# Kernel optimization log

Hardware: AMD Instinct MI355X
Metric: run time of the kernel (lower is better)

## Reference

```python
import jax, jax.numpy as jnp
import numpy as np

# NVFP4 E2M1 representable magnitudes and decision midpoints (round-to-nearest)
_E2M1_GRID = np.array([0.0, 0.5, 1.0, 1.5, 2.0, 3.0, 4.0, 6.0], dtype=np.float32)
_E2M1_MIDS = np.array([0.25, 0.75, 1.25, 1.75, 2.5, 3.5, 5.0], dtype=np.float32)
_BLOCK = 16  # quant_tile_shape=(1,16)


def fake_quant_nvfp4(t):
    """Blockwise (16 contiguous elems) E2M1 fake quant with pow2 scales."""
    shape = t.shape
    v = t.reshape(-1, _BLOCK)                      # [n_blocks, 16]
    amax = jnp.max(jnp.abs(v), axis=-1, keepdims=True)
    # power-of-2 scale so that amax/scale <= 6 (E2M1 max)
    exp = jnp.ceil(jnp.log2(jnp.maximum(amax, jnp.float32(1e-30)) / 6.0))
    scale = jnp.where(amax > 0, jnp.exp2(exp), jnp.float32(1.0))
    u = v / scale
    a = jnp.abs(u)
    grid = jnp.asarray(_E2M1_GRID, dtype=t.dtype)
    mids = jnp.asarray(_E2M1_MIDS, dtype=t.dtype)
    idx = jnp.digitize(a, mids)                    # nearest E2M1 magnitude index
    q = jnp.sign(u) * grid[idx]
    return (q * scale).reshape(shape)


def setup_inputs() -> dict:
    key = jax.random.key(0)
    kx, kw = jax.random.split(key)
    x = jax.random.normal(kx, (32, 256, 64, 64), dtype=jnp.float32)
    w = jax.random.normal(kw, (256, 256, 3, 3), dtype=jnp.float32) * 0.05
    return {"x": x, "w": w}


def reference(x, w):
    qx = fake_quant_nvfp4(x)
    qw = fake_quant_nvfp4(w)
    # conv2d, stride 1, padding 1, no bias, NCHW / OIHW
    return jax.lax.conv_general_dilated(
        qx, qw,
        window_strides=(1, 1),
        padding=((1, 1), (1, 1)),
        dimension_numbers=("NCHW", "OIHW", "NCHW"),
    )
```

## Files before the change

kernel.cpp:

```cpp
#include <hip/hip_runtime.h>
#include <stdint.h>

typedef __attribute__((ext_vector_type(8))) short short8;
typedef __attribute__((ext_vector_type(4))) float f32x4;

#define N_IMG 32
#define C_IN  256
#define HH    64
#define WW    64
#define O_OUT 256
#define HP    66
#define WP    66

#define QX_ELEMS (N_IMG*HP*WP*C_IN)
#define QX_BYTES ((size_t)QX_ELEMS*2)
#define QW_ELEMS (9*O_OUT*C_IN)


__device__ __forceinline__ float e2m1_mag(float a) {
    return a < 0.25f ? 0.0f
         : a < 0.75f ? 0.5f
         : a < 1.25f ? 1.0f
         : a < 1.75f ? 1.5f
         : a < 2.5f  ? 2.0f
         : a < 3.5f  ? 3.0f
         : a < 5.0f  ? 4.0f : 6.0f;
}

__device__ __forceinline__ void blk_scale2(float amax, float& s, float& inv) {
    float ac = fmaxf(amax, 1e-30f);
    int e;
    float m = frexpf(ac, &e);
    int ex = (m > 0.75f) ? (e - 2) : (e - 3);
    if (amax > 0.0f) { s = ldexpf(1.0f, ex); inv = ldexpf(1.0f, -ex); }
    else             { s = 1.0f; inv = 1.0f; }
}

__device__ __forceinline__ unsigned short to_bf16_bits(float v) {
    union { float f; unsigned int u; } cv; cv.f = v;
    return (unsigned short)(cv.u >> 16);
}

__global__ __launch_bounds__(256) void halo_zero_kernel(unsigned short* __restrict__ qx) {
    int id = blockIdx.x * 256 + threadIdx.x;
    size_t off;
    if (id < 135168) {
        int n = id / 4224, r = id % 4224;
        int h = (r / 2112) * 65;
        int k = r % 2112;
        off = (((size_t)(n*HP + h)) * WP) * C_IN + (size_t)k * 8;
    } else {
        int j = id - 135168;
        int n = j >> 12, r = j & 4095;
        int h = 1 + (r >> 6);
        int w = ((r >> 5) & 1) * 65;
        int k = r & 31;
        off = (((size_t)(n*HP + h)) * WP + w) * C_IN + (size_t)k * 8;
    }
    uint4 z; z.x = z.y = z.z = z.w = 0u;
    *(uint4*)(qx + off) = z;
}

__global__ __launch_bounds__(256) void quant_x_kernel(const float* __restrict__ x,
                                                      unsigned short* __restrict__ qx) {
    __shared__ float xf[64][65];
    __shared__ float sarr[4][65];
    __shared__ float iarr[4][65];

    const int bid = blockIdx.x;
    const int n  = bid >> 8;
    const int h  = (bid >> 2) & 63;
    const int cb = bid & 3;
    const int t  = threadIdx.x;

    {
        const int rb = t >> 4;
        const int w4 = (t & 15) * 4;
        const float* src = x + (((size_t)(n*C_IN + cb*64)) * HH + h) * WW;
#pragma unroll
        for (int it = 0; it < 4; ++it) {
            int r = it * 16 + rb;
            float4 g = *(const float4*)(src + (size_t)r * (HH*WW) + w4);
            xf[r][w4+0] = g.x; xf[r][w4+1] = g.y; xf[r][w4+2] = g.z; xf[r][w4+3] = g.w;
        }
    }
    __syncthreads();

    {
        const int c = t >> 2, wb = t & 3;
        float amax = 0.f;
#pragma unroll
        for (int j = 0; j < 16; ++j) amax = fmaxf(amax, fabsf(xf[c][wb*16 + j]));
        float s, inv;
        blk_scale2(amax, s, inv);
        sarr[wb][c] = s;
        iarr[wb][c] = inv;
    }
    __syncthreads();

    {
        const int w = t >> 2, cg = (t & 3) * 16, wb = w >> 4;
        unsigned short outv[16];
#pragma unroll
        for (int i = 0; i < 16; ++i) {
            int c = cg + i;
            float v = xf[c][w];
            float q = copysignf(e2m1_mag(fabsf(v) * iarr[wb][c]) * sarr[wb][c], v);
            outv[i] = to_bf16_bits(q);
        }
        unsigned short* dst = qx + (((size_t)(n*HP + h + 1)) * WP + (w + 1)) * C_IN + cb*64 + cg;
        *(uint4*)(dst)     = *(const uint4*)&outv[0];
        *(uint4*)(dst + 8) = *(const uint4*)&outv[8];
    }
}

__global__ __launch_bounds__(256) void quant_w_kernel(const float* __restrict__ w,
                                                      unsigned short* __restrict__ qw) {
    __shared__ unsigned short lq[2304];
    const int o = blockIdx.x;
    const int t = threadIdx.x;
    const float* src = w + (size_t)o * 2304;
    if (t < 144) {
        float v[16];
#pragma unroll
        for (int j = 0; j < 4; ++j) {
            float4 f = ((const float4*)(src + t*16))[j];
            v[j*4+0]=f.x; v[j*4+1]=f.y; v[j*4+2]=f.z; v[j*4+3]=f.w;
        }
        float amax = 0.f;
#pragma unroll
        for (int j = 0; j < 16; ++j) amax = fmaxf(amax, fabsf(v[j]));
        float s, inv;
        blk_scale2(amax, s, inv);
#pragma unroll
        for (int j = 0; j < 16; ++j)
            lq[t*16 + j] = to_bf16_bits(copysignf(e2m1_mag(fabsf(v[j]) * inv) * s, v[j]));
    }
    __syncthreads();
#pragma unroll
    for (int p = 0; p < 9; ++p)
        qw[((size_t)(p*O_OUT + o)) * C_IN + t] = lq[t*9 + p];
}

__device__ __forceinline__ void gld16(void* lds, const void* g) {
    __builtin_amdgcn_global_load_lds(
        (const __attribute__((address_space(1))) unsigned int*)g,
        (__attribute__((address_space(3))) unsigned int*)lds,
        16, 0, 0);
}

__global__ __launch_bounds__(256) void conv_kernel(const unsigned short* __restrict__ qw,
                                                   const unsigned short* __restrict__ qx,
                                                   float* __restrict__ out) {
    __shared__ unsigned short Wt[128][32];
    __shared__ unsigned short Xt[128][32];

    const int tid  = threadIdx.x;
    const int wave = tid >> 6;
    const int lane = tid & 63;
    const int lo16 = lane & 15;
    const int quad = lane >> 4;

    const int id  = blockIdx.x;
    const int g   = id >> 3;
    const int n   = ((g >> 6) << 3) | (id & 7);
    const int j_  = g & 63;
    const int o0  = (j_ & 1) * 128;
    const int hw0 = (j_ >> 1) * 128;
    const int h0  = hw0 >> 6;

    const int s0 = wave * 2;
    const int r0 = s0 * 16 + (lane >> 2);
    const int r1 = r0 + 16;
    const int co = (lane & 3) * 8;

    const unsigned short* wb0 = qw + (size_t)(o0 + r0) * C_IN + co;
    const unsigned short* wb1 = qw + (size_t)(o0 + r1) * C_IN + co;

    auto xbase = [&](int r) -> const unsigned short* {
        int h = h0 + (r >> 6);
        int w = r & 63;
        return qx + (((size_t)(n*HP + h + 1)) * WP + (w + 1)) * C_IN + co;
    };
    const unsigned short* xb0 = xbase(r0);
    const unsigned short* xb1 = xbase(r1);

    unsigned short* ldsA0 = &Wt[s0*16][0];
    unsigned short* ldsA1 = &Wt[s0*16 + 16][0];
    unsigned short* ldsB0 = &Xt[s0*16][0];
    unsigned short* ldsB1 = &Xt[s0*16 + 16][0];

    const int wmo = (wave & 1) * 64;
    const int wnp = (wave >> 1) * 64;

    f32x4 acc[4][4];
#pragma unroll
    for (int i = 0; i < 4; ++i)
#pragma unroll
        for (int j = 0; j < 4; ++j)
            acc[i][j] = (f32x4){0.f, 0.f, 0.f, 0.f};

    for (int p = 0; p < 9; ++p) {
        const int dh = p/3 - 1, dw = p%3 - 1;
        const int xoff = (dh*WP + dw) * C_IN;
        const int woff = p * (O_OUT * C_IN);
        for (int cc = 0; cc < 8; ++cc) {
            const int c0 = cc * 32;
            gld16(ldsA0, wb0 + woff + c0);
            gld16(ldsA1, wb1 + woff + c0);
            gld16(ldsB0, xb0 + xoff + c0);
            gld16(ldsB1, xb1 + xoff + c0);
            __syncthreads();

            short8 af[4], bf_[4];
#pragma unroll
            for (int i = 0; i < 4; ++i)
                af[i] = *(const short8*)&Wt[wmo + i*16 + lo16][quad*8];
#pragma unroll
            for (int j = 0; j < 4; ++j)
                bf_[j] = *(const short8*)&Xt[wnp + j*16 + lo16][quad*8];
#pragma unroll
            for (int i = 0; i < 4; ++i)
#pragma unroll
                for (int j = 0; j < 4; ++j)
                    acc[i][j] = __builtin_amdgcn_mfma_f32_16x16x32_bf16(
                        af[i], bf_[j], acc[i][j], 0, 0, 0);
            __syncthreads();
        }
    }

#pragma unroll
    for (int i = 0; i < 4; ++i) {
#pragma unroll
        for (int j = 0; j < 4; ++j) {
            int o  = o0 + wmo + i*16 + quad*4;
            int pl = wnp + j*16 + lo16;
            size_t base = ((size_t)(n*O_OUT + o)) * (HH*WW) + hw0 + pl;
#pragma unroll
            for (int r = 0; r < 4; ++r)
                out[base + (size_t)r*(HH*WW)] = acc[i][j][r];
        }
    }
}

extern "C" void kernel_launch(void* const* d_in, const int* in_sizes, int n_in,
                              void* d_out, int out_size, void* d_ws, size_t ws_size,
                              hipStream_t stream) {
    const float* x = (const float*)d_in[0];
    const float* w = (const float*)d_in[1];
    float* out = (float*)d_out;

    unsigned short* qx = (unsigned short*)d_ws;
    unsigned short* qw = (unsigned short*)((char*)d_ws + QX_BYTES);

    halo_zero_kernel<<<dim3(1040), 256, 0, stream>>>(qx);
    quant_x_kernel<<<dim3(N_IMG*HH*4), 256, 0, stream>>>(x, qx);
    quant_w_kernel<<<dim3(O_OUT), 256, 0, stream>>>(w, qw);
    conv_kernel<<<dim3(2048), 256, 0, stream>>>(qw, qx, out);
}
```

Measured before the change: 433.4 us.

## Double-buffer X tile in LDS, load weights directly to registers, swizzle LDS

Measured after the change: 543.0 us. 25.3% more time.

```diff
diff --git a/kernel.cpp b/kernel.cpp
--- a/kernel.cpp
+++ b/kernel.cpp
@@ -139,7 +139,7 @@
     __syncthreads();
 #pragma unroll
     for (int p = 0; p < 9; ++p)
-        qw[((size_t)(p*O_OUT + o)) * C_IN + t] = lq[t*9 + p];
+        qw[(size_t)o*2304 + p*C_IN + t] = lq[t*9 + p];
 }
 
 __device__ __forceinline__ void gld16(void* lds, const void* g) {
@@ -152,8 +152,7 @@
 __global__ __launch_bounds__(256) void conv_kernel(const unsigned short* __restrict__ qw,
                                                    const unsigned short* __restrict__ qx,
                                                    float* __restrict__ out) {
-    __shared__ unsigned short Wt[128][32];
-    __shared__ unsigned short Xt[128][32];
+    __shared__ unsigned short Xb[2][128][32];
 
     const int tid  = threadIdx.x;
     const int wave = tid >> 6;
@@ -169,29 +168,25 @@
     const int hw0 = (j_ >> 1) * 128;
     const int h0  = hw0 >> 6;
 
-    const int s0 = wave * 2;
-    const int r0 = s0 * 16 + (lane >> 2);
+    const int r0 = wave*32 + (lane >> 2);
     const int r1 = r0 + 16;
-    const int co = (lane & 3) * 8;
-
-    const unsigned short* wb0 = qw + (size_t)(o0 + r0) * C_IN + co;
-    const unsigned short* wb1 = qw + (size_t)(o0 + r1) * C_IN + co;
-
-    auto xbase = [&](int r) -> const unsigned short* {
-        int h = h0 + (r >> 6);
-        int w = r & 63;
-        return qx + (((size_t)(n*HP + h + 1)) * WP + (w + 1)) * C_IN + co;
-    };
-    const unsigned short* xb0 = xbase(r0);
-    const unsigned short* xb1 = xbase(r1);
-
-    unsigned short* ldsA0 = &Wt[s0*16][0];
-    unsigned short* ldsA1 = &Wt[s0*16 + 16][0];
-    unsigned short* ldsB0 = &Xt[s0*16][0];
-    unsigned short* ldsB1 = &Xt[s0*16 + 16][0];
+    const int cl = (lane & 3) ^ ((lane >> 3) & 3);
+    const int co = cl * 8;
+
+    const unsigned short* xb0 = qx + (((size_t)(n*HP + h0 + (r0 >> 6) + 1))*WP + (r0 & 63) + 1)*C_IN + co;
+    const unsigned short* xb1 = qx + (((size_t)(n*HP + h0 + (r1 >> 6) + 1))*WP + (r1 & 63) + 1)*C_IN + co;
+
+    unsigned short* ldsB0[2] = { &Xb[0][wave*32][0],      &Xb[1][wave*32][0] };
+    unsigned short* ldsB1[2] = { &Xb[0][wave*32 + 16][0], &Xb[1][wave*32 + 16][0] };
 
     const int wmo = (wave & 1) * 64;
     const int wnp = (wave >> 1) * 64;
+    const unsigned short* ap[4];
+#pragma unroll
+    for (int i = 0; i < 4; ++i)
+        ap[i] = qw + (size_t)(o0 + wmo + i*16 + lo16) * 2304 + quad*8;
+
+    const int pq8 = (quad ^ ((lo16 >> 1) & 3)) * 8;
 
     f32x4 acc[4][4];
 #pragma unroll
@@ -200,33 +195,49 @@
         for (int j = 0; j < 4; ++j)
             acc[i][j] = (f32x4){0.f, 0.f, 0.f, 0.f};
 
+    short8 areg[2][4];
+
+    const int XO0 = -17152;
+    gld16(ldsB0[0], xb0 + XO0);
+    gld16(ldsB1[0], xb1 + XO0);
+#pragma unroll
+    for (int i = 0; i < 4; ++i) areg[0][i] = *(const short8*)(ap[i]);
+
+    int xo = XO0;
     for (int p = 0; p < 9; ++p) {
-        const int dh = p/3 - 1, dw = p%3 - 1;
-        const int xoff = (dh*WP + dw) * C_IN;
-        const int woff = p * (O_OUT * C_IN);
+        const int xo_n = xo + (((p == 2) | (p == 5)) ? 64*256 : 256);
+        const int pb   = p * 256;
+#pragma unroll
         for (int cc = 0; cc < 8; ++cc) {
-            const int c0 = cc * 32;
-            gld16(ldsA0, wb0 + woff + c0);
-            gld16(ldsA1, wb1 + woff + c0);
-            gld16(ldsB0, xb0 + xoff + c0);
-            gld16(ldsB1, xb1 + xoff + c0);
+            const int cur = cc & 1;
+            const int nxt = cur ^ 1;
             __syncthreads();
-
-            short8 af[4], bf_[4];
-#pragma unroll
-            for (int i = 0; i < 4; ++i)
-                af[i] = *(const short8*)&Wt[wmo + i*16 + lo16][quad*8];
+            if (cc < 7) {
+                const int bo = xo + (cc + 1) * 32;
+                gld16(ldsB0[nxt], xb0 + bo);
+                gld16(ldsB1[nxt], xb1 + bo);
+                const int ao = pb + (cc + 1) * 32;
+#pragma unroll
+                for (int i = 0; i < 4; ++i) areg[nxt][i] = *(const short8*)(ap[i] + ao);
+            } else if (p < 8) {
+                gld16(ldsB0[nxt], xb0 + xo_n);
+                gld16(ldsB1[nxt], xb1 + xo_n);
+                const int ao = pb + 256;
+#pragma unroll
+                for (int i = 0; i < 4; ++i) areg[nxt][i] = *(const short8*)(ap[i] + ao);
+            }
+            short8 bf_[4];
 #pragma unroll
             for (int j = 0; j < 4; ++j)
-                bf_[j] = *(const short8*)&Xt[wnp + j*16 + lo16][quad*8];
+                bf_[j] = *(const short8*)&Xb[cur][wnp + j*16 + lo16][pq8];
 #pragma unroll
             for (int i = 0; i < 4; ++i)
 #pragma unroll
                 for (int j = 0; j < 4; ++j)
                     acc[i][j] = __builtin_amdgcn_mfma_f32_16x16x32_bf16(
-                        af[i], bf_[j], acc[i][j], 0, 0, 0);
-            __syncthreads();
-        }
+                        areg[cur][i], bf_[j], acc[i][j], 0, 0, 0);
+        }
+        xo = xo_n;
     }
 
 #pragma unroll
```
